# Kernel optimization log

Hardware: AMD Instinct MI355X
Metric: run time of the kernel (lower is better)

## Reference

```python
import jax, jax.numpy as jnp
import numpy as np

B, C, H, W = 4, 256, 64, 64


def setup_inputs() -> dict:
    key = jax.random.key(0)
    ks = jax.random.split(key, 7)
    s = 1.0 / np.sqrt(C)
    return {
        "x": jax.random.normal(ks[0], (B, C, H, W), jnp.float32),
        "context": jax.random.normal(ks[1], (B, C, H, W), jnp.float32),
        "wq": jax.random.normal(ks[2], (C, C), jnp.float32) * s,
        "bq": jnp.zeros((C,), jnp.float32),
        "wk": jax.random.normal(ks[3], (C, C), jnp.float32) * s,
        "bk": jnp.zeros((C,), jnp.float32),
        "wv": jax.random.normal(ks[4], (C, C), jnp.float32) * s,
        "bv": jnp.zeros((C,), jnp.float32),
        "wo": jax.random.normal(ks[5], (C, C), jnp.float32) * s,
        "bo": jnp.zeros((C,), jnp.float32),
    }


def _proj(w, b, feats):
    # 1x1 conv == channel-mixing linear: feats [B,C,N] -> [B,C,N]
    return jnp.einsum("oc,bcn->bon", w, feats) + b[None, :, None]


def reference(x, context, wq, bq, wk, bk, wv, bv, wo, bo):
    b, c, h, w = x.shape
    xf = x.reshape(b, c, h * w)              # [B,C,Nq]
    cf = context.reshape(b, c, -1)           # [B,C,Nk]
    q = _proj(wq, bq, xf)                    # [B,C,Nq]
    k = _proj(wk, bk, cf)                    # [B,C,Nk]
    v = _proj(wv, bv, cf)                    # [B,C,Nk]
    attn = jnp.einsum("bci,bcj->bij", q, k)  # [B,Nq,Nk] = q^T k
    attn = jax.nn.softmax(attn, axis=-1)
    out = jnp.einsum("bcj,bij->bci", v, attn)  # v @ attn^T, [B,C,Nq]
    out = _proj(wo, bo, out).reshape(b, c, h, w)
    return out + x
```

## Files before the change

### kernel.cpp

```cpp
#include <hip/hip_runtime.h>

typedef __bf16 bf16x8 __attribute__((ext_vector_type(8)));
typedef float f32x4 __attribute__((ext_vector_type(4)));
typedef unsigned short us4 __attribute__((ext_vector_type(4)));
typedef unsigned short us8 __attribute__((ext_vector_type(8)));
typedef unsigned short u16;

#define DEVI __device__ __forceinline__

constexpr int B_ = 4, C_ = 256, N_ = 4096;

DEVI u16 f2bf(float f) {
  unsigned u = __builtin_bit_cast(unsigned, f);
  u += 0x7fffu + ((u >> 16) & 1u);
  return (u16)(u >> 16);
}
DEVI float bf2f(u16 h) { return __builtin_bit_cast(float, ((unsigned)h) << 16); }

#define MFMA16(a, b, c) __builtin_amdgcn_mfma_f32_16x16x32_bf16((a), (b), (c), 0, 0, 0)

DEVI void gload16(const void* g, void* l) {
  __builtin_amdgcn_global_load_lds((const __attribute__((address_space(1))) void*)g,
                                   (__attribute__((address_space(3))) void*)l, 16, 0, 0);
}

DEVI float bcast_row(float v0, float v1, float v2, float v3, int l15) {
  int src = (l15 >> 2) << 4;
  float a0 = __shfl(v0, src, 64);
  float a1 = __shfl(v1, src, 64);
  float a2 = __shfl(v2, src, 64);
  float a3 = __shfl(v3, src, 64);
  float x0 = (l15 & 1) ? a1 : a0;
  float x1 = (l15 & 1) ? a3 : a2;
  return (l15 & 2) ? x1 : x0;
}

__global__ __launch_bounds__(256, 1) void prep_weights(
    const float* __restrict__ wq, const float* __restrict__ wk,
    const float* __restrict__ wv, const float* __restrict__ wo,
    u16* __restrict__ wqh, u16* __restrict__ wql,
    u16* __restrict__ wkh, u16* __restrict__ wkl,
    u16* __restrict__ wvh, u16* __restrict__ woh) {
  int idx = blockIdx.x * 256 + threadIdx.x;
  float q = wq[idx];
  u16 qh = f2bf(q);
  wqh[idx] = qh;
  wql[idx] = f2bf(q - bf2f(qh));
  float k = wk[idx];
  u16 kh = f2bf(k);
  wkh[idx] = kh;
  wkl[idx] = f2bf(k - bf2f(kh));
  wvh[idx] = f2bf(wv[idx]);
  woh[idx] = f2bf(wo[idx]);
}

__global__ __launch_bounds__(256, 2) void proj_kv(
    const float* __restrict__ ctx, const float* __restrict__ bk, const float* __restrict__ bv,
    const u16* __restrict__ wkh, const u16* __restrict__ wkl, const u16* __restrict__ wvh,
    u16* __restrict__ KTh, u16* __restrict__ Vg) {
  const int blk = blockIdx.x;
  const int b = blk & 3;
  const int j0 = (blk >> 2) << 6;
  const int tid = threadIdx.x;
  const int lane = tid & 63;
  const int w = tid >> 6;
  const int l15 = lane & 15;
  const int g = lane >> 4;

  __shared__ alignas(16) u16 ldsH[64 * 256];
  __shared__ alignas(16) u16 ldsL[64 * 256];

  {
    const float* cb = ctx + (size_t)b * C_ * N_ + j0;
    #pragma unroll
    for (int it = 0; it < 16; ++it) {
      int idx = it * 256 + tid;
      int c = idx >> 4;
      int j4 = (idx & 15) << 2;
      float4 f = *(const float4*)(cb + (size_t)c * N_ + j4);
      float vv[4] = {f.x, f.y, f.z, f.w};
      #pragma unroll
      for (int e = 0; e < 4; ++e) {
        int j = j4 + e;
        u16 h = f2bf(vv[e]);
        int uidx = j * 256 + ((((c >> 3) ^ (j & 7))) << 3) + (c & 7);
        ldsH[uidx] = h;
        ldsL[uidx] = f2bf(vv[e] - bf2f(h));
      }
    }
  }
  __syncthreads();

  const int jloc = 16 * w + l15;
  bf16x8 ch[8], cl[8];
  #pragma unroll
  for (int ks = 0; ks < 8; ++ks) {
    int uidx = jloc * 256 + (((g + 4 * ks) ^ (jloc & 7)) << 3);
    ch[ks] = *(const bf16x8*)&ldsH[uidx];
    cl[ks] = *(const bf16x8*)&ldsL[uidx];
  }

  #pragma unroll 4
  for (int mt = 0; mt < 16; ++mt) {
    f32x4 ka = {0, 0, 0, 0}, ka2 = {0, 0, 0, 0}, va = {0, 0, 0, 0};
    #pragma unroll
    for (int ks = 0; ks < 8; ++ks) {
      int aoff = (16 * mt + l15) * 256 + 8 * g + 32 * ks;
      bf16x8 ah = *(const bf16x8*)(wkh + aoff);
      bf16x8 al = *(const bf16x8*)(wkl + aoff);
      bf16x8 av = *(const bf16x8*)(wvh + aoff);
      ka = MFMA16(ah, ch[ks], ka);
      ka2 = MFMA16(ah, cl[ks], ka2);
      ka2 = MFMA16(al, ch[ks], ka2);
      va = MFMA16(av, ch[ks], va);
    }
    int c0 = 16 * mt + 4 * g;
    float4 bk4 = *(const float4*)(bk + c0);
    float4 bv4 = *(const float4*)(bv + c0);
    us4 h4;
    #pragma unroll
    for (int r = 0; r < 4; ++r) h4[r] = f2bf(ka[r] + ka2[r] + ((const float*)&bk4)[r]);
    *(us4*)(KTh + ((size_t)b * N_ + j0 + jloc) * C_ + c0) = h4;
    #pragma unroll
    for (int r = 0; r < 4; ++r) {
      float vv = va[r] + ((const float*)&bv4)[r];
      Vg[((size_t)b * C_ + c0 + r) * N_ + j0 + jloc] = f2bf(vv);
    }
  }
}

DEVI void stageK(const u16* khg, int kv0, u16* ldsK, int w, int lane) {
  #pragma unroll
  for (int t = 0; t < 8; ++t) {
    int L = t * 256 + w * 64 + lane;
    int j = L >> 5, s = L & 31;
    const u16* src = khg + (size_t)(kv0 + j) * C_ + ((s ^ (j & 7)) << 3);
    gload16(src, ldsK + (size_t)(t * 256 + w * 64) * 8);
  }
}
DEVI void stageV(const u16* vg, int kv0, u16* ldsV, int w, int lane) {
  #pragma unroll
  for (int t = 0; t < 8; ++t) {
    int L = t * 256 + w * 64 + lane;
    int c = L >> 3, sl = L & 7;
    const u16* src = vg + (size_t)c * N_ + kv0 + ((sl ^ (c & 7)) << 3);
    gload16(src, ldsV + (size_t)(t * 256 + w * 64) * 8);
  }
}

__global__ __launch_bounds__(256, 2) void attn_fused(
    const float* __restrict__ x, const float* __restrict__ bq, const float* __restrict__ bo,
    const u16* __restrict__ wqh, const u16* __restrict__ wql, const u16* __restrict__ woh,
    const u16* __restrict__ KTh, const u16* __restrict__ Vg,
    float* __restrict__ out) {
  const int blk = blockIdx.x;
  const int b = (blk & 7) >> 1;
  const int i0 = (((blk >> 3) << 1) | (blk & 1)) << 6;
  const int tid = threadIdx.x;
  const int lane = tid & 63;
  const int w = tid >> 6;
  const int l15 = lane & 15;
  const int g = lane >> 4;

  __shared__ alignas(16) char smem[74752];
  u16* ldsK = (u16*)smem;
  u16* ldsV = (u16*)(smem + 32768);
  u16* ldsPT = (u16*)(smem + 65536);

  {
    const float* xb = x + (size_t)b * C_ * N_ + i0;
    #pragma unroll
    for (int it = 0; it < 16; ++it) {
      int idx = it * 256 + tid;
      int c = idx >> 4;
      int i4 = (idx & 15) << 2;
      float4 f = *(const float4*)(xb + (size_t)c * N_ + i4);
      float vv[4] = {f.x, f.y, f.z, f.w};
      #pragma unroll
      for (int e = 0; e < 4; ++e) {
        int i = i4 + e;
        u16 h = f2bf(vv[e]);
        int uidx = i * 256 + ((((c >> 3) ^ (i & 7))) << 3) + (c & 7);
        ldsK[uidx] = h;
        ldsV[uidx] = f2bf(vv[e] - bf2f(h));
      }
    }
  }
  __syncthreads();

  const int iloc = 16 * w + l15;

  bf16x8 xh[8], xl[8];
  #pragma unroll
  for (int ks = 0; ks < 8; ++ks) {
    int uidx = iloc * 256 + (((g + 4 * ks) ^ (iloc & 7)) << 3);
    xh[ks] = *(const bf16x8*)&ldsK[uidx];
    xl[ks] = *(const bf16x8*)&ldsV[uidx];
  }

  f32x4 qd[16];
  #pragma unroll
  for (int mt = 0; mt < 16; ++mt) {
    f32x4 a1 = {0, 0, 0, 0}, a2 = {0, 0, 0, 0};
    #pragma unroll
    for (int ks = 0; ks < 8; ++ks) {
      int aoff = (16 * mt + l15) * 256 + 8 * g + 32 * ks;
      bf16x8 ah = *(const bf16x8*)(wqh + aoff);
      bf16x8 al = *(const bf16x8*)(wql + aoff);
      a1 = MFMA16(ah, xh[ks], a1);
      a2 = MFMA16(ah, xl[ks], a2);
      a2 = MFMA16(al, xh[ks], a2);
    }
    int c0 = 16 * mt + 4 * g;
    float4 bq4 = *(const float4*)(bq + c0);
    #pragma unroll
    for (int r = 0; r < 4; ++r) qd[mt][r] = a1[r] + a2[r] + ((const float*)&bq4)[r];
  }
  __syncthreads();

  #pragma unroll
  for (int mt = 0; mt < 16; ++mt) {
    int c0 = 16 * mt + 4 * g;
    us4 h4, l4;
    #pragma unroll
    for (int r = 0; r < 4; ++r) {
      u16 hh = f2bf(qd[mt][r]);
      h4[r] = hh;
      l4[r] = f2bf(qd[mt][r] - bf2f(hh));
    }
    int uidx = iloc * 256 + ((((c0 >> 3) ^ (iloc & 7))) << 3) + (c0 & 7);
    *(us4*)&ldsK[uidx] = h4;
    *(us4*)&ldsV[uidx] = l4;
  }
  __syncthreads();

  bf16x8 qh[8], ql[8];
  #pragma unroll
  for (int ks = 0; ks < 8; ++ks) {
    int uidx = iloc * 256 + (((g + 4 * ks) ^ (iloc & 7)) << 3);
    qh[ks] = *(const bf16x8*)&ldsK[uidx];
    ql[ks] = *(const bf16x8*)&ldsV[uidx];
  }
  __syncthreads();

  const u16* khg = KTh + (size_t)b * N_ * C_;
  const u16* vg = Vg + (size_t)b * C_ * N_;

  stageK(khg, 0, ldsK, w, lane);
  stageV(vg, 0, ldsV, w, lane);

  float mrun[4] = {-1e30f, -1e30f, -1e30f, -1e30f};
  float lrun[4] = {0, 0, 0, 0};
  f32x4 oacc[16];
  #pragma unroll
  for (int mt = 0; mt < 16; ++mt) oacc[mt] = (f32x4){0, 0, 0, 0};

  __syncthreads();

  for (int kv0 = 0; kv0 < N_; kv0 += 64) {
    f32x4 s1[4], s2[4];
    #pragma unroll
    for (int nt = 0; nt < 4; ++nt) {
      s1[nt] = (f32x4){0, 0, 0, 0};
      s2[nt] = (f32x4){0, 0, 0, 0};
    }
    #pragma unroll
    for (int ks = 0; ks < 8; ++ks) {
      bf16x8 bh[4];
      #pragma unroll
      for (int nt = 0; nt < 4; ++nt) {
        int j = 16 * nt + l15;
        bh[nt] = *(const bf16x8*)&ldsK[j * 256 + (((g + 4 * ks) ^ (j & 7)) << 3)];
      }
      #pragma unroll
      for (int nt = 0; nt < 4; ++nt) s1[nt] = MFMA16(qh[ks], bh[nt], s1[nt]);
      #pragma unroll
      for (int nt = 0; nt < 4; ++nt) s2[nt] = MFMA16(ql[ks], bh[nt], s2[nt]);
    }
    #pragma unroll
    for (int nt = 0; nt < 4; ++nt) s1[nt] += s2[nt];

    float tm[4];
    #pragma unroll
    for (int r = 0; r < 4; ++r) {
      tm[r] = fmaxf(fmaxf(s1[0][r], s1[1][r]), fmaxf(s1[2][r], s1[3][r]));
      #pragma unroll
      for (int msk = 1; msk < 16; msk <<= 1) tm[r] = fmaxf(tm[r], __shfl_xor(tm[r], msk));
    }
    bool grow = (tm[0] > mrun[0] + 6.f) | (tm[1] > mrun[1] + 6.f) |
                (tm[2] > mrun[2] + 6.f) | (tm[3] > mrun[3] + 6.f);
    float sc[4];
    int need = __any((int)grow);
    if (need) {
      #pragma unroll
      for (int r = 0; r < 4; ++r) {
        float mn = fmaxf(mrun[r], tm[r]);
        sc[r] = __expf(mrun[r] - mn);
        mrun[r] = mn;
      }
      float fsc = bcast_row(sc[0], sc[1], sc[2], sc[3], l15);
      #pragma unroll
      for (int mt = 0; mt < 16; ++mt) oacc[mt] *= fsc;
    }
    float rs[4] = {0, 0, 0, 0};
    #pragma unroll
    for (int nt = 0; nt < 4; ++nt) {
      #pragma unroll
      for (int r = 0; r < 4; ++r) {
        float p = __expf(s1[nt][r] - mrun[r]);
        s1[nt][r] = p;
        rs[r] += p;
      }
    }
    #pragma unroll
    for (int r = 0; r < 4; ++r) {
      #pragma unroll
      for (int msk = 1; msk < 16; msk <<= 1) rs[r] += __shfl_xor(rs[r], msk);
      lrun[r] = need ? lrun[r] * sc[r] + rs[r] : lrun[r] + rs[r];
    }

    #pragma unroll
    for (int nt = 0; nt < 4; ++nt) {
      int jcol = 16 * nt + l15;
      #pragma unroll
      for (int r = 0; r < 4; ++r) ldsPT[w * 1152 + (4 * g + r) * 72 + jcol] = f2bf(s1[nt][r]);
    }

    __syncthreads();
    if (kv0 + 64 < N_) stageK(khg, kv0 + 64, ldsK, w, lane);

    bf16x8 pb[2];
    #pragma unroll
    for (int ks2 = 0; ks2 < 2; ++ks2)
      pb[ks2] = *(const bf16x8*)&ldsPT[w * 1152 + l15 * 72 + 8 * (g + 4 * ks2)];
    #pragma unroll
    for (int ks2 = 0; ks2 < 2; ++ks2) {
      #pragma unroll
      for (int mt = 0; mt < 16; ++mt) {
        int c = 16 * mt + l15;
        bf16x8 va = *(const bf16x8*)&ldsV[c * 64 + (((g + 4 * ks2) ^ (c & 7)) << 3)];
        oacc[mt] = MFMA16(va, pb[ks2], oacc[mt]);
      }
    }

    __syncthreads();
    if (kv0 + 64 < N_) stageV(vg, kv0 + 64, ldsV, w, lane);
  }

  {
    float inv[4];
    #pragma unroll
    for (int r = 0; r < 4; ++r) inv[r] = 1.0f / lrun[r];
    float fi = bcast_row(inv[0], inv[1], inv[2], inv[3], l15);
    #pragma unroll
    for (int mt = 0; mt < 16; ++mt) oacc[mt] *= fi;
  }
  #pragma unroll
  for (int mt = 0; mt < 16; ++mt) {
    int c0 = 16 * mt + 4 * g;
    us4 h4;
    #pragma unroll
    for (int r = 0; r < 4; ++r) h4[r] = f2bf(oacc[mt][r]);
    int uidx = iloc * 256 + ((((c0 >> 3) ^ (iloc & 7))) << 3) + (c0 & 7);
    *(us4*)&ldsK[uidx] = h4;
  }
  f32x4 facc[16];
  #pragma unroll
  for (int mt = 0; mt < 16; ++mt) facc[mt] = (f32x4){0, 0, 0, 0};
  #pragma unroll
  for (int ks = 0; ks < 8; ++ks) {
    bf16x8 ob = *(const bf16x8*)&ldsK[iloc * 256 + (((g + 4 * ks) ^ (iloc & 7)) << 3)];
    #pragma unroll
    for (int mt = 0; mt < 16; ++mt) {
      bf16x8 ah = *(const bf16x8*)(woh + (16 * mt + l15) * 256 + 8 * g + 32 * ks);
      facc[mt] = MFMA16(ah, ob, facc[mt]);
    }
  }
  const int ig = i0 + iloc;
  #pragma unroll
  for (int mt = 0; mt < 16; ++mt) {
    int c0 = 16 * mt + 4 * g;
    float4 bo4 = *(const float4*)(bo + c0);
    #pragma unroll
    for (int r = 0; r < 4; ++r) {
      size_t off = ((size_t)b * C_ + c0 + r) * N_ + ig;
      out[off] = facc[mt][r] + ((const float*)&bo4)[r] + x[off];
    }
  }
}

extern "C" void kernel_launch(void* const* d_in, const int* in_sizes, int n_in,
                              void* d_out, int out_size, void* d_ws, size_t ws_size,
                              hipStream_t stream) {
  const float* x = (const float*)d_in[0];
  const float* ctx = (const float*)d_in[1];
  const float* wq = (const float*)d_in[2];
  const float* bq = (const float*)d_in[3];
  const float* wk = (const float*)d_in[4];
  const float* bk = (const float*)d_in[5];
  const float* wv = (const float*)d_in[6];
  const float* bv = (const float*)d_in[7];
  const float* wo = (const float*)d_in[8];
  const float* bo = (const float*)d_in[9];
  float* out = (float*)d_out;

  u16* ws = (u16*)d_ws;
  u16* wqh = ws;
  u16* wql = wqh + 65536;
  u16* wkh = wql + 65536;
  u16* wkl = wkh + 65536;
  u16* wvh = wkl + 65536;
  u16* woh = wvh + 65536;
  u16* KTh = woh + 65536;
  u16* Vg = KTh + (size_t)B_ * N_ * C_;

  prep_weights<<<256, 256, 0, stream>>>(wq, wk, wv, wo, wqh, wql, wkh, wkl, wvh, woh);
  proj_kv<<<256, 256, 0, stream>>>(ctx, bk, bv, wkh, wkl, wvh, KTh, Vg);
  attn_fused<<<256, 256, 0, stream>>>(x, bq, bo, wqh, wql, woh, KTh, Vg, out);
}
```

Measured before the change: 397.5 us.

## Switch to fp16 MFMA without hi/lo split and double-buffer K/V tiles

Replaces the bf16 hi+lo split-precision scheme with single fp16 operands throughout. This drops the extra correction MFMAs in the Q/K projections and in the QK^T score computation, along with the extra LDS traffic for low parts. The attention loop now double-buffers K and V in LDS, prefetching the next tile while computing the current one, and needs only one barrier per iteration. LDS use roughly doubles, so occupancy falls to one block per CU, and fp16 range and precision may risk accuracy on the scores.

```diff
diff --git a/kernel.cpp b/kernel.cpp
--- a/kernel.cpp
+++ b/kernel.cpp
@@ -1,23 +1,15 @@
 #include <hip/hip_runtime.h>
 
-typedef __bf16 bf16x8 __attribute__((ext_vector_type(8)));
+typedef _Float16 f16;
+typedef _Float16 f16x8 __attribute__((ext_vector_type(8)));
+typedef _Float16 f16x4 __attribute__((ext_vector_type(4)));
 typedef float f32x4 __attribute__((ext_vector_type(4)));
-typedef unsigned short us4 __attribute__((ext_vector_type(4)));
-typedef unsigned short us8 __attribute__((ext_vector_type(8)));
-typedef unsigned short u16;
 
 #define DEVI __device__ __forceinline__
 
 constexpr int B_ = 4, C_ = 256, N_ = 4096;
 
-DEVI u16 f2bf(float f) {
-  unsigned u = __builtin_bit_cast(unsigned, f);
-  u += 0x7fffu + ((u >> 16) & 1u);
-  return (u16)(u >> 16);
-}
-DEVI float bf2f(u16 h) { return __builtin_bit_cast(float, ((unsigned)h) << 16); }
-
-#define MFMA16(a, b, c) __builtin_amdgcn_mfma_f32_16x16x32_bf16((a), (b), (c), 0, 0, 0)
+#define MFMAH(a, b, c) __builtin_amdgcn_mfma_f32_16x16x32_f16((a), (b), (c), 0, 0, 0)
 
 DEVI void gload16(const void* g, void* l) {
   __builtin_amdgcn_global_load_lds((const __attribute__((address_space(1))) void*)g,
@@ -38,26 +30,19 @@
 __global__ __launch_bounds__(256, 1) void prep_weights(
     const float* __restrict__ wq, const float* __restrict__ wk,
     const float* __restrict__ wv, const float* __restrict__ wo,
-    u16* __restrict__ wqh, u16* __restrict__ wql,
-    u16* __restrict__ wkh, u16* __restrict__ wkl,
-    u16* __restrict__ wvh, u16* __restrict__ woh) {
+    f16* __restrict__ wqh, f16* __restrict__ wkh,
+    f16* __restrict__ wvh, f16* __restrict__ woh) {
   int idx = blockIdx.x * 256 + threadIdx.x;
-  float q = wq[idx];
-  u16 qh = f2bf(q);
-  wqh[idx] = qh;
-  wql[idx] = f2bf(q - bf2f(qh));
-  float k = wk[idx];
-  u16 kh = f2bf(k);
-  wkh[idx] = kh;
-  wkl[idx] = f2bf(k - bf2f(kh));
-  wvh[idx] = f2bf(wv[idx]);
-  woh[idx] = f2bf(wo[idx]);
+  wqh[idx] = (f16)wq[idx];
+  wkh[idx] = (f16)wk[idx];
+  wvh[idx] = (f16)wv[idx];
+  woh[idx] = (f16)wo[idx];
 }
 
 __global__ __launch_bounds__(256, 2) void proj_kv(
     const float* __restrict__ ctx, const float* __restrict__ bk, const float* __restrict__ bv,
-    const u16* __restrict__ wkh, const u16* __restrict__ wkl, const u16* __restrict__ wvh,
-    u16* __restrict__ KTh, u16* __restrict__ Vg) {
+    const f16* __restrict__ wkh, const f16* __restrict__ wvh,
+    f16* __restrict__ KTh, f16* __restrict__ Vg) {
   const int blk = blockIdx.x;
   const int b = blk & 3;
   const int j0 = (blk >> 2) << 6;
@@ -67,8 +52,7 @@
   const int l15 = lane & 15;
   const int g = lane >> 4;
 
-  __shared__ alignas(16) u16 ldsH[64 * 256];
-  __shared__ alignas(16) u16 ldsL[64 * 256];
+  __shared__ alignas(16) f16 ldsC[64 * 256];
 
   {
     const float* cb = ctx + (size_t)b * C_ * N_ + j0;
@@ -82,76 +66,68 @@
       #pragma unroll
       for (int e = 0; e < 4; ++e) {
         int j = j4 + e;
-        u16 h = f2bf(vv[e]);
         int uidx = j * 256 + ((((c >> 3) ^ (j & 7))) << 3) + (c & 7);
-        ldsH[uidx] = h;
-        ldsL[uidx] = f2bf(vv[e] - bf2f(h));
+        ldsC[uidx] = (f16)vv[e];
       }
     }
   }
   __syncthreads();
 
   const int jloc = 16 * w + l15;
-  bf16x8 ch[8], cl[8];
-  #pragma unroll
-  for (int ks = 0; ks < 8; ++ks) {
-    int uidx = jloc * 256 + (((g + 4 * ks) ^ (jloc & 7)) << 3);
-    ch[ks] = *(const bf16x8*)&ldsH[uidx];
-    cl[ks] = *(const bf16x8*)&ldsL[uidx];
-  }
+  f16x8 ch[8];
+  #pragma unroll
+  for (int ks = 0; ks < 8; ++ks)
+    ch[ks] = *(const f16x8*)&ldsC[jloc * 256 + (((g + 4 * ks) ^ (jloc & 7)) << 3)];
 
   #pragma unroll 4
   for (int mt = 0; mt < 16; ++mt) {
-    f32x4 ka = {0, 0, 0, 0}, ka2 = {0, 0, 0, 0}, va = {0, 0, 0, 0};
+    f32x4 ka = {0, 0, 0, 0}, va = {0, 0, 0, 0};
     #pragma unroll
     for (int ks = 0; ks < 8; ++ks) {
       int aoff = (16 * mt + l15) * 256 + 8 * g + 32 * ks;
-      bf16x8 ah = *(const bf16x8*)(wkh + aoff);
-      bf16x8 al = *(const bf16x8*)(wkl + aoff);
-      bf16x8 av = *(const bf16x8*)(wvh + aoff);
-      ka = MFMA16(ah, ch[ks], ka);
-      ka2 = MFMA16(ah, cl[ks], ka2);
-      ka2 = MFMA16(al, ch[ks], ka2);
-      va = MFMA16(av, ch[ks], va);
+      f16x8 ah = *(const f16x8*)(wkh + aoff);
+      f16x8 av = *(const f16x8*)(wvh + aoff);
+      ka = MFMAH(ah, ch[ks], ka);
+      va = MFMAH(av, ch[ks], va);
     }
     int c0 = 16 * mt + 4 * g;
     float4 bk4 = *(const float4*)(bk + c0);
     float4 bv4 = *(const float4*)(bv + c0);
-    us4 h4;
-    #pragma unroll
-    for (int r = 0; r < 4; ++r) h4[r] = f2bf(ka[r] + ka2[r] + ((const float*)&bk4)[r]);
-    *(us4*)(KTh + ((size_t)b * N_ + j0 + jloc) * C_ + c0) = h4;
+    f16x4 h4;
+    #pragma unroll
+    for (int r = 0; r < 4; ++r) h4[r] = (f16)(ka[r] + ((const float*)&bk4)[r]);
+    *(f16x4*)(KTh + ((size_t)b * N_ + j0 + jloc) * C_ + c0) = h4;
     #pragma unroll
     for (int r = 0; r < 4; ++r) {
       float vv = va[r] + ((const float*)&bv4)[r];
-      Vg[((size_t)b * C_ + c0 + r) * N_ + j0 + jloc] = f2bf(vv);
-    }
-  }
-}
-
-DEVI void stageK(const u16* khg, int kv0, u16* ldsK, int w, int lane) {
+      Vg[((size_t)b * C_ + c0 + r) * N_ + j0 + jloc] = (f16)vv;
+    }
+  }
+}
+
+DEVI void stageK(const f16* khg, int kv0, f16* ldsK, int w, int lane) {
   #pragma unroll
   for (int t = 0; t < 8; ++t) {
     int L = t * 256 + w * 64 + lane;
     int j = L >> 5, s = L & 31;
-    const u16* src = khg + (size_t)(kv0 + j) * C_ + ((s ^ (j & 7)) << 3);
+    const f16* src = khg + (size_t)(kv0 + j) * C_ + ((s ^ (j & 7)) << 3);
     gload16(src, ldsK + (size_t)(t * 256 + w * 64) * 8);
   }
 }
-DEVI void stageV(const u16* vg, int kv0, u16* ldsV, int w, int lane) {
+DEVI void stageV(const f16* vg, int kv0, f16* ldsV, int w, int lane) {
   #pragma unroll
   for (int t = 0; t < 8; ++t) {
     int L = t * 256 + w * 64 + lane;
     int c = L >> 3, sl = L & 7;
-    const u16* src = vg + (size_t)c * N_ + kv0 + ((sl ^ (c & 7)) << 3);
+    const f16* src = vg + (size_t)c * N_ + kv0 + ((sl ^ (c & 7)) << 3);
     gload16(src, ldsV + (size_t)(t * 256 + w * 64) * 8);
   }
 }
 
-__global__ __launch_bounds__(256, 2) void attn_fused(
+__global__ __launch_bounds__(256, 1) void attn_fused(
     const float* __restrict__ x, const float* __restrict__ bq, const float* __restrict__ bo,
-    const u16* __restrict__ wqh, const u16* __restrict__ wql, const u16* __restrict__ woh,
-    const u16* __restrict__ KTh, const u16* __restrict__ Vg,
+    const f16* __restrict__ wqh, const f16* __restrict__ woh,
+    const f16* __restrict__ KTh, const f16* __restrict__ Vg,
     float* __restrict__ out) {
   const int blk = blockIdx.x;
   const int b = (blk & 7) >> 1;
@@ -162,10 +138,12 @@
   const int l15 = lane & 15;
   const int g = lane >> 4;
 
-  __shared__ alignas(16) char smem[74752];
-  u16* ldsK = (u16*)smem;
-  u16* ldsV = (u16*)(smem + 32768);
-  u16* ldsPT = (u16*)(smem + 65536);
+  __shared__ alignas(16) char smem[140288];
+  f16* ldsK0 = (f16*)smem;
+  f16* ldsK1 = (f16*)(smem + 32768);
+  f16* ldsV0 = (f16*)(smem + 65536);
+  f16* ldsV1 = (f16*)(smem + 98304);
+  f16* ldsPT = (f16*)(smem + 131072);
 
   {
     const float* xb = x + (size_t)b * C_ * N_ + i0;
@@ -179,10 +157,8 @@
       #pragma unroll
       for (int e = 0; e < 4; ++e) {
         int i = i4 + e;
-        u16 h = f2bf(vv[e]);
         int uidx = i * 256 + ((((c >> 3) ^ (i & 7))) << 3) + (c & 7);
-        ldsK[uidx] = h;
-        ldsV[uidx] = f2bf(vv[e] - bf2f(h));
+        ldsK0[uidx] = (f16)vv[e];
       }
     }
   }
@@ -190,64 +166,45 @@
 
   const int iloc = 16 * w + l15;
 
-  bf16x8 xh[8], xl[8];
-  #pragma unroll
-  for (int ks = 0; ks < 8; ++ks) {
-    int uidx = iloc * 256 + (((g + 4 * ks) ^ (iloc & 7)) << 3);
-    xh[ks] = *(const bf16x8*)&ldsK[uidx];
-    xl[ks] = *(const bf16x8*)&ldsV[uidx];
-  }
+  f16x8 xh[8];
+  #pragma unroll
+  for (int ks = 0; ks < 8; ++ks)
+    xh[ks] = *(const f16x8*)&ldsK0[iloc * 256 + (((g + 4 * ks) ^ (iloc & 7)) << 3)];
 
   f32x4 qd[16];
   #pragma unroll
   for (int mt = 0; mt < 16; ++mt) {
-    f32x4 a1 = {0, 0, 0, 0}, a2 = {0, 0, 0, 0};
+    f32x4 a1 = {0, 0, 0, 0};
     #pragma unroll
     for (int ks = 0; ks < 8; ++ks) {
-      int aoff = (16 * mt + l15) * 256 + 8 * g + 32 * ks;
-      bf16x8 ah = *(const bf16x8*)(wqh + aoff);
-      bf16x8 al = *(const bf16x8*)(wql + aoff);
-      a1 = MFMA16(ah, xh[ks], a1);
-      a2 = MFMA16(ah, xl[ks], a2);
-      a2 = MFMA16(al, xh[ks], a2);
+      f16x8 ah = *(const f16x8*)(wqh + (16 * mt + l15) * 256 + 8 * g + 32 * ks);
+      a1 = MFMAH(ah, xh[ks], a1);
     }
     int c0 = 16 * mt + 4 * g;
     float4 bq4 = *(const float4*)(bq + c0);
     #pragma unroll
-    for (int r = 0; r < 4; ++r) qd[mt][r] = a1[r] + a2[r] + ((const float*)&bq4)[r];
-  }
-  __syncthreads();
-
-  #pragma unroll
-  for (int mt = 0; mt < 16; ++mt) {
-    int c0 = 16 * mt + 4 * g;
-    us4 h4, l4;
-    #pragma unroll
-    for (int r = 0; r < 4; ++r) {
-      u16 hh = f2bf(qd[mt][r]);
-      h4[r] = hh;
-      l4[r] = f2bf(qd[mt][r] - bf2f(hh));
-    }
-    int uidx = iloc * 256 + ((((c0 >> 3) ^ (iloc & 7))) << 3) + (c0 & 7);
-    *(us4*)&ldsK[uidx] = h4;
-    *(us4*)&ldsV[uidx] = l4;
-  }
-  __syncthreads();
-
-  bf16x8 qh[8], ql[8];
-  #pragma unroll
-  for (int ks = 0; ks < 8; ++ks) {
-    int uidx = iloc * 256 + (((g + 4 * ks) ^ (iloc & 7)) << 3);
-    qh[ks] = *(const bf16x8*)&ldsK[uidx];
-    ql[ks] = *(const bf16x8*)&ldsV[uidx];
-  }
-  __syncthreads();
-
-  const u16* khg = KTh + (size_t)b * N_ * C_;
-  const u16* vg = Vg + (size_t)b * C_ * N_;
-
-  stageK(khg, 0, ldsK, w, lane);
-  stageV(vg, 0, ldsV, w, lane);
+    for (int r = 0; r < 4; ++r) qd[mt][r] = a1[r] + ((const float*)&bq4)[r];
+  }
+  __syncthreads();
+
+  #pragma unroll
+  for (int mt = 0; mt < 16; ++mt) {
+    int c0 = 16 * mt + 4 * g;
+    f16x4 h4;
+    #pragma unroll
+    for (int r = 0; r < 4; ++r) h4[r] = (f16)qd[mt][r];
+    *(f16x4*)&ldsK0[iloc * 256 + ((((c0 >> 3) ^ (iloc & 7))) << 3) + (c0 & 7)] = h4;
+  }
+  __syncthreads();
+
+  f16x8 qh[8];
+  #pragma unroll
+  for (int ks = 0; ks < 8; ++ks)
+    qh[ks] = *(const f16x8*)&ldsK0[iloc * 256 + (((g + 4 * ks) ^ (iloc & 7)) << 3)];
+  __syncthreads();
+
+  const f16* khg = KTh + (size_t)b * N_ * C_;
+  const f16* vg = Vg + (size_t)b * C_ * N_;
 
   float mrun[4] = {-1e30f, -1e30f, -1e30f, -1e30f};
   float lrun[4] = {0, 0, 0, 0};
@@ -255,30 +212,36 @@
   #pragma unroll
   for (int mt = 0; mt < 16; ++mt) oacc[mt] = (f32x4){0, 0, 0, 0};
 
-  __syncthreads();
-
-  for (int kv0 = 0; kv0 < N_; kv0 += 64) {
-    f32x4 s1[4], s2[4];
-    #pragma unroll
-    for (int nt = 0; nt < 4; ++nt) {
-      s1[nt] = (f32x4){0, 0, 0, 0};
-      s2[nt] = (f32x4){0, 0, 0, 0};
-    }
+  stageK(khg, 0, ldsK0, w, lane);
+  stageV(vg, 0, ldsV0, w, lane);
+  __syncthreads();
+
+  for (int t = 0; t < 64; ++t) {
+    const int kv0 = t << 6;
+    f16* Kc = (t & 1) ? ldsK1 : ldsK0;
+    f16* Vc = (t & 1) ? ldsV1 : ldsV0;
+    f16* Kn = (t & 1) ? ldsK0 : ldsK1;
+    f16* Vn = (t & 1) ? ldsV0 : ldsV1;
+
+    if (t < 63) {
+      stageK(khg, kv0 + 64, Kn, w, lane);
+      stageV(vg, kv0 + 64, Vn, w, lane);
+    }
+
+    f32x4 s1[4];
+    #pragma unroll
+    for (int nt = 0; nt < 4; ++nt) s1[nt] = (f32x4){0, 0, 0, 0};
     #pragma unroll
     for (int ks = 0; ks < 8; ++ks) {
-      bf16x8 bh[4];
+      f16x8 bh[4];
       #pragma unroll
       for (int nt = 0; nt < 4; ++nt) {
         int j = 16 * nt + l15;
-        bh[nt] = *(const bf16x8*)&ldsK[j * 256 + (((g + 4 * ks) ^ (j & 7)) << 3)];
-      }
-      #pragma unroll
-      for (int nt = 0; nt < 4; ++nt) s1[nt] = MFMA16(qh[ks], bh[nt], s1[nt]);
-      #pragma unroll
-      for (int nt = 0; nt < 4; ++nt) s2[nt] = MFMA16(ql[ks], bh[nt], s2[nt]);
-    }
-    #pragma unroll
-    for (int nt = 0; nt < 4; ++nt) s1[nt] += s2[nt];
+        bh[nt] = *(const f16x8*)&Kc[j * 256 + (((g + 4 * ks) ^ (j & 7)) << 3)];
+      }
+      #pragma unroll
+      for (int nt = 0; nt < 4; ++nt) s1[nt] = MFMAH(qh[ks], bh[nt], s1[nt]);
+    }
 
     float tm[4];
     #pragma unroll
@@ -289,7 +252,7 @@
     }
     bool grow = (tm[0] > mrun[0] + 6.f) | (tm[1] > mrun[1] + 6.f) |
                 (tm[2] > mrun[2] + 6.f) | (tm[3] > mrun[3] + 6.f);
-    float sc[4];
+    float sc[4] = {1.f, 1.f, 1.f, 1.f};
     int need = __any((int)grow);
     if (need) {
       #pragma unroll
@@ -323,28 +286,24 @@
     for (int nt = 0; nt < 4; ++nt) {
       int jcol = 16 * nt + l15;
       #pragma unroll
-      for (int r = 0; r < 4; ++r) ldsPT[w * 1152 + (4 * g + r) * 72 + jcol] = f2bf(s1[nt][r]);
-    }
-
-    __syncthreads();
-    if (kv0 + 64 < N_) stageK(khg, kv0 + 64, ldsK, w, lane);
-
-    bf16x8 pb[2];
+      for (int r = 0; r < 4; ++r) ldsPT[w * 1152 + (4 * g + r) * 72 + jcol] = (f16)s1[nt][r];
+    }
+    f16x8 pb[2];
     #pragma unroll
     for (int ks2 = 0; ks2 < 2; ++ks2)
-      pb[ks2] = *(const bf16x8*)&ldsPT[w * 1152 + l15 * 72 + 8 * (g + 4 * ks2)];
+      pb[ks2] = *(const f16x8*)&ldsPT[w * 1152 + l15 * 72 + 8 * (g + 4 * ks2)];
+
     #pragma unroll
     for (int ks2 = 0; ks2 < 2; ++ks2) {
       #pragma unroll
       for (int mt = 0; mt < 16; ++mt) {
         int c = 16 * mt + l15;
-        bf16x8 va = *(const bf16x8*)&ldsV[c * 64 + (((g + 4 * ks2) ^ (c & 7)) << 3)];
-        oacc[mt] = MFMA16(va, pb[ks2], oacc[mt]);
+        f16x8 va = *(const f16x8*)&Vc[c * 64 + (((g + 4 * ks2) ^ (c & 7)) << 3)];
+        oacc[mt] = MFMAH(va, pb[ks2], oacc[mt]);
       }
     }
 
     __syncthreads();
-    if (kv0 + 64 < N_) stageV(vg, kv0 + 64, ldsV, w, lane);
   }
 
   {
@@ -358,22 +317,22 @@
   #pragma unroll
   for (int mt = 0; mt < 16; ++mt) {
     int c0 = 16 * mt + 4 * g;
-    us4 h4;
-    #pragma unroll
-    for (int r = 0; r < 4; ++r) h4[r] = f2bf(oacc[mt][r]);
-    int uidx = iloc * 256 + ((((c0 >> 3) ^ (iloc & 7))) << 3) + (c0 & 7);
-    *(us4*)&ldsK[uidx] = h4;
-  }
+    f16x4 h4;
+    #pragma unroll
+    for (int r = 0; r < 4; ++r) h4[r] = (f16)oacc[mt][r];
+    *(f16x4*)&ldsK0[iloc * 256 + ((((c0 >> 3) ^ (iloc & 7))) << 3) + (c0 & 7)] = h4;
+  }
+  __syncthreads();
   f32x4 facc[16];
   #pragma unroll
   for (int mt = 0; mt < 16; ++mt) facc[mt] = (f32x4){0, 0, 0, 0};
   #pragma unroll
   for (int ks = 0; ks < 8; ++ks) {
-    bf16x8 ob = *(const bf16x8*)&ldsK[iloc * 256 + (((g + 4 * ks) ^ (iloc & 7)) << 3)];
+    f16x8 ob = *(const f16x8*)&ldsK0[iloc * 256 + (((g + 4 * ks) ^ (iloc & 7)) << 3)];
     #pragma unroll
     for (int mt = 0; mt < 16; ++mt) {
-      bf16x8 ah = *(const bf16x8*)(woh + (16 * mt + l15) * 256 + 8 * g + 32 * ks);
-      facc[mt] = MFMA16(ah, ob, facc[mt]);
+      f16x8 ah = *(const f16x8*)(woh + (16 * mt + l15) * 256 + 8 * g + 32 * ks);
+      facc[mt] = MFMAH(ah, ob, facc[mt]);
     }
   }
   const int ig = i0 + iloc;
@@ -404,17 +363,15 @@
   const float* bo = (const float*)d_in[9];
   float* out = (float*)d_out;
 
-  u16* ws = (u16*)d_ws;
-  u16* wqh = ws;
-  u16* wql = wqh + 65536;
-  u16* wkh = wql + 65536;
-  u16* wkl = wkh + 65536;
-  u16* wvh = wkl + 65536;
-  u16* woh = wvh + 65536;
-  u16* KTh = woh + 65536;
-  u16* Vg = KTh + (size_t)B_ * N_ * C_;
-
-  prep_weights<<<256, 256, 0, stream>>>(wq, wk, wv, wo, wqh, wql, wkh, wkl, wvh, woh);
-  proj_kv<<<256, 256, 0, stream>>>(ctx, bk, bv, wkh, wkl, wvh, KTh, Vg);
-  attn_fused<<<256, 256, 0, stream>>>(x, bq, bo, wqh, wql, woh, KTh, Vg, out);
-}
+  f16* ws = (f16*)d_ws;
+  f16* wqh = ws;
+  f16* wkh = wqh + 65536;
+  f16* wvh = wkh + 65536;
+  f16* woh = wvh + 65536;
+  f16* KTh = woh + 65536;
+  f16* Vg = KTh + (size_t)B_ * N_ * C_;
+
+  prep_weights<<<256, 256, 0, stream>>>(wq, wk, wv, wo, wqh, wkh, wvh, woh);
+  proj_kv<<<256, 256, 0, stream>>>(ctx, bk, bv, wkh, wvh, KTh, Vg);
+  attn_fused<<<256, 256, 0, stream>>>(x, bq, bo, wqh, woh, KTh, Vg, out);
+}
```

Result: faster. 354.6 us (-10.8%).
